# Kernel tuning notes

Hardware: AMD Instinct MI355X
Metric: run time of the kernel (lower is better)

## Reference

```python
import jax, jax.numpy as jnp
import numpy as np
from jax import lax

BASE = 10000.0

def _rope(x):
    # x: (b, h, w, c). Faithful to torch RoPE: angles depend only on one spatial
    # axis (h,k_max) and broadcast against the *w* axis of x (valid since h==w).
    b, h, w, c = x.shape
    k_max = c // 2
    theta = 1.0 / (BASE ** (jnp.arange(k_max, dtype=x.dtype) / k_max))  # (k_max,)
    angles = jnp.arange(h, dtype=x.dtype)[:, None] * theta              # (h, k_max)
    cos = jnp.cos(angles)[None, None]  # (1,1,h,k_max) -> broadcasts over w axis
    sin = jnp.sin(angles)[None, None]
    xr = x.reshape(b, h, w, k_max, 2)
    re, im = xr[..., 0], xr[..., 1]
    out = jnp.stack([re * cos - im * sin, re * sin + im * cos], axis=-1)
    return out.reshape(b, h, w, c)


def setup_inputs() -> dict:
    key = jax.random.key(0)
    k1, k2, k3 = jax.random.split(key, 3)
    B, C, H, W = 8, 128, 160, 160
    x = jax.random.normal(k1, (B, C, H, W), dtype=jnp.float32)
    qk_w = jax.random.normal(k2, (2 * C, C), dtype=jnp.float32) * 0.02
    qk_b = jnp.zeros((2 * C,), dtype=jnp.float32)
    lepe_w = jax.random.normal(k3, (C, 1, 3, 3), dtype=jnp.float32) * 0.1
    lepe_b = jnp.zeros((C,), dtype=jnp.float32)
    return {"x": x, "qk_w": qk_w, "qk_b": qk_b,
            "lepe_w": lepe_w, "lepe_b": lepe_b, "num_heads": 8}


def reference(x, qk_w, qk_b, lepe_w, lepe_b, num_heads):
    b, c, H, W = x.shape
    n = H * W
    hd = c // num_heads
    # raw row-major reshape (B,C,H,W) -> (B,N,C), matching torch .reshape
    xf = x.reshape(b, n, c)
    qk = (xf @ qk_w.T + qk_b).reshape(b, n, 2, c)
    q = jax.nn.elu(qk[:, :, 0]) + 1.0
    k = jax.nn.elu(qk[:, :, 1]) + 1.0
    v = xf
    q_rope = _rope(q.reshape(b, H, W, c)).reshape(b, n, num_heads, hd).transpose(0, 2, 1, 3)
    k_rope = _rope(k.reshape(b, H, W, c)).reshape(b, n, num_heads, hd).transpose(0, 2, 1, 3)
    qh = q.reshape(b, n, num_heads, hd).transpose(0, 2, 1, 3)  # (b,h,n,d)
    kh = k.reshape(b, n, num_heads, hd).transpose(0, 2, 1, 3)
    vh = v.reshape(b, n, num_heads, hd).transpose(0, 2, 1, 3)
    z = 1.0 / (jnp.einsum('bhnd,bhd->bhn', qh, kh.mean(axis=2)) + 1e-6)  # (b,h,n)
    scale = float(n) ** -0.5
    kv = jnp.einsum('bhnd,bhne->bhde', k_rope * scale, vh * scale)  # (b,h,d,d)
    out = jnp.einsum('bhnd,bhde->bhne', q_rope, kv) * z[..., None]  # (b,h,n,d)
    out = out.transpose(0, 2, 1, 3).reshape(b, n, c)
    # LePE: depthwise 3x3 conv on v laid out as image
    vimg = vh.transpose(0, 2, 1, 3).reshape(b, H, W, c).transpose(0, 3, 1, 2)  # (b,c,H,W)
    lepe = lax.conv_general_dilated(vimg, lepe_w, (1, 1), 'SAME',
                                    feature_group_count=c)
    lepe = lepe + lepe_b[None, :, None, None]
    out = out + lepe.transpose(0, 2, 3, 1).reshape(b, n, c)
    return out.transpose(0, 2, 1).reshape(b, c, H, W)
```

## Files before the change

kernel.cpp:

```cpp
#include <hip/hip_runtime.h>
#include <cstdint>
#include <cstddef>

#define NB 8
#define NC 128
#define NHH 160
#define NWW 160
#define NNN (NHH*NWW)
#define TILE_R 64
#define TPB (NNN/TILE_R)
#define NSLOTS 32
#define LN_B 0.14391156511f

typedef __attribute__((ext_vector_type(8))) short short8v;
typedef __attribute__((ext_vector_type(4))) short short4v;
typedef __attribute__((ext_vector_type(4))) float f32x4;
union B64x2 { short8v v8; short4v v4[2]; ushort u[8]; uint w[4]; };

__device__ __forceinline__ float elup1(float y){ return y>0.f? y+1.f : __expf(y); }
__device__ __forceinline__ ushort f2bf(float f){ uint x=__float_as_uint(f); x+=0x7fffu+((x>>16)&1u); return (ushort)(x>>16); }
__device__ __forceinline__ uint cvtpk(float lo, float hi){
  uint r;
  asm("v_cvt_pk_bf16_f32 %0, %1, %2" : "=v"(r) : "v"(lo), "v"(hi));
  return r;
}
__device__ __forceinline__ float frcp(float x){
  float r;
  asm("v_rcp_f32 %0, %1" : "=v"(r) : "v"(x));
  return r;
}
__device__ __forceinline__ float bfhi(uint u){ return __uint_as_float(u & 0xffff0000u); }
__device__ __forceinline__ float bflo(uint u){ return __uint_as_float(u << 16); }
__device__ __forceinline__ int divH(int i){ return ((i >> 5) * 6554) >> 15; }
__device__ __forceinline__ int iclamp(int v, int lo, int hi){ return v<lo?lo:(v>hi?hi:v); }

__global__ __launch_bounds__(256) void kprep(
    const float* __restrict__ qk_w, ushort* __restrict__ wbf,
    float2* __restrict__ rtab, float* __restrict__ zreg)
{
  const int id = blockIdx.x*256 + threadIdx.x;
  if (id < 2*NC*NC) wbf[id] = f2bf(qk_w[id]);
  if (id < NWW*64) {
    const int ww = id >> 6, f = id & 63;
    const float th = __expf(-LN_B * (float)f);
    float s, c; __sincosf((float)ww * th, &s, &c);
    rtab[id] = make_float2(c, s);
  }
  #pragma unroll
  for (int j = 0; j < 17; ++j)
    zreg[id + j*32768] = 0.f;
}

__global__ __launch_bounds__(256, 3) void k1_proj(
    const float* __restrict__ x, const ushort* __restrict__ wbf,
    const float* __restrict__ qk_b, const float2* __restrict__ rtab,
    float* __restrict__ kv_part, float* __restrict__ ksum_part)
{
  __shared__ __align__(16) ushort xbf[64][136];
  __shared__ __align__(16) ushort wch[64][136];
  __shared__ __align__(16) ushort xtp[64][68];
  __shared__ __align__(16) ushort krt[64][68];
  __shared__ float ksum_lds[NC];

  const int blk  = ((blockIdx.x & 7) * (NB*TPB/8)) + (blockIdx.x >> 3);
  const int b    = blk / TPB;
  const int tile = blk - b * TPB;
  const int i0   = tile * TILE_R;
  const int tid  = threadIdx.x;
  const int lane = tid & 63;
  const int wv   = tid >> 6;
  const int lg   = lane >> 4;
  const int ll   = lane & 15;
  const float* xb = x + (size_t)b*NNN*NC + (size_t)i0*NC;

  {
    const float4* src = (const float4*)xb;
    for (int f = tid; f < TILE_R*NC/4; f += 256) {
      float4 v = src[f];
      uint w0 = cvtpk(v.x, v.y), w1 = cvtpk(v.z, v.w);
      *(uint2*)&xbf[f >> 5][(f & 31) << 2] = make_uint2(w0, w1);
    }
  }
  if (tid < NC) ksum_lds[tid] = 0.f;
  __syncthreads();

  f32x4 kvacc[2];
  kvacc[0] = (f32x4){0.f,0.f,0.f,0.f};
  kvacc[1] = (f32x4){0.f,0.f,0.f,0.f};
  const int row0 = (wv<<4) + (lg<<2);

  int wfr4[4];
  #pragma unroll
  for (int r = 0; r < 4; ++r) {
    const int i = i0 + row0 + r;
    wfr4[r] = i - divH(i)*NWW;
  }

  for (int chunk = 0; chunk < 2; ++chunk) {
    if (chunk) __syncthreads();
    {
      const uint4* wsrc = (const uint4*)(wbf + (size_t)(NC + chunk*64)*NC);
      for (int f = tid; f < 1024; f += 256)
        *(uint4*)&wch[f >> 4][(f & 15) << 3] = wsrc[f];
    }
    {
      #pragma unroll
      for (int t = 0; t < 2; ++t) {
        const int task = tid + (t << 8);
        const int c = task & 63, rg = task >> 6;
        ushort tmp[8];
        #pragma unroll
        for (int k2 = 0; k2 < 8; ++k2) tmp[k2] = xbf[(rg<<3)+k2][(chunk<<6)+c];
        *(ushort4*)&xtp[c][(rg<<3)]   = make_ushort4(tmp[0],tmp[1],tmp[2],tmp[3]);
        *(ushort4*)&xtp[c][(rg<<3)+4] = make_ushort4(tmp[4],tmp[5],tmp[6],tmp[7]);
      }
    }
    __syncthreads();

    f32x4 acc[4];
    acc[0]=acc[1]=acc[2]=acc[3]=(f32x4){0.f,0.f,0.f,0.f};
    #pragma unroll
    for (int ks = 0; ks < 4; ++ks) {
      short8v a = *(const short8v*)&xbf[(wv<<4) + ll][(ks<<5) + (lg<<3)];
      #pragma unroll
      for (int nt = 0; nt < 4; ++nt) {
        short8v bb = *(const short8v*)&wch[(nt<<4) + ll][(ks<<5) + (lg<<3)];
        acc[nt] = __builtin_amdgcn_mfma_f32_16x16x32_bf16(a, bb, acc[nt], 0, 0, 0);
      }
    }

    #pragma unroll
    for (int nt = 0; nt < 4; ++nt) {
      const int kcl = (nt<<4) + ll;
      const int kc  = (chunk<<6) + kcl;
      const float bias = qk_b[NC + kc];
      float kk[4]; float ss = 0.f;
      #pragma unroll
      for (int r = 0; r < 4; ++r) { kk[r] = elup1(acc[nt][r] + bias); ss += kk[r]; }
      atomicAdd(&ksum_lds[kc], ss);
      ushort rb[4];
      #pragma unroll
      for (int r = 0; r < 4; ++r) {
        float p = __shfl_xor(kk[r], 1);
        float2 cs = rtab[wfr4[r]*64 + (kc >> 1)];
        float kr = (kc & 1) ? (p*cs.y + kk[r]*cs.x) : (kk[r]*cs.x - p*cs.y);
        rb[r] = f2bf(kr);
      }
      *(uint*)&krt[kcl][row0]   = (uint)rb[0] | ((uint)rb[1] << 16);
      *(uint*)&krt[kcl][row0+2] = (uint)rb[2] | ((uint)rb[3] << 16);
    }
    __syncthreads();

    #pragma unroll
    for (int ks = 0; ks < 2; ++ks) {
      const int rb2 = (ks<<5) + (lg<<3);
      B64x2 ua, ub;
      ua.v4[0] = *(const short4v*)&krt[(wv<<4) + ll][rb2];
      ua.v4[1] = *(const short4v*)&krt[(wv<<4) + ll][rb2+4];
      ub.v4[0] = *(const short4v*)&xtp[(wv<<4) + ll][rb2];
      ub.v4[1] = *(const short4v*)&xtp[(wv<<4) + ll][rb2+4];
      kvacc[chunk] = __builtin_amdgcn_mfma_f32_16x16x32_bf16(ua.v8, ub.v8, kvacc[chunk], 0, 0, 0);
    }
  }

  const int slot = blk & (NSLOTS-1);
  {
    float* kvp = kv_part + ((size_t)b*NSLOTS + slot) * 2048;
    #pragma unroll
    for (int e2 = 0; e2 < 2; ++e2) {
      const int h = (e2<<2) + wv;
      #pragma unroll
      for (int r = 0; r < 4; ++r) {
        const int d = (lg<<2) + r;
        atomicAdd(&kvp[(h<<8) + (d<<4) + ll], kvacc[e2][r]);
      }
    }
  }
  if (tid < NC) atomicAdd(&ksum_part[((size_t)b*NSLOTS + slot)*NC + tid], ksum_lds[tid]);
}

__global__ __launch_bounds__(256) void k_reduce(
    const float* __restrict__ kv_part, const float* __restrict__ ksum_part,
    float* __restrict__ kvf, float* __restrict__ kmean)
{
  const int gtid = blockIdx.x * 256 + threadIdx.x;
  const int b = gtid >> 11;
  const int cidx = gtid & 2047;
  float s = 0.f;
  for (int sl = 0; sl < NSLOTS; ++sl)
    s += kv_part[((size_t)b*NSLOTS + sl)*2048 + cidx];
  kvf[(size_t)b*2048 + cidx] = s * (1.f/25600.f);
  if (cidx < NC) {
    float t = 0.f;
    for (int sl = 0; sl < NSLOTS; ++sl)
      t += ksum_part[((size_t)b*NSLOTS + sl)*NC + cidx];
    kmean[(size_t)b*NC + cidx] = t * (1.f/25600.f);
  }
}

__global__ __launch_bounds__(256, 2) void k2_out(
    const float* __restrict__ x, const ushort* __restrict__ wbf,
    const float* __restrict__ qk_b, const float* __restrict__ kvf,
    const float* __restrict__ kmean, const float* __restrict__ lepe_w,
    const float* __restrict__ lepe_b, const float2* __restrict__ rtab,
    float* __restrict__ outp)
{
  __shared__ __align__(16) ushort qu_s[64*136];

  const int blk  = ((blockIdx.x & 7) * (NB*TPB/8)) + (blockIdx.x >> 3);
  const int b    = blk / TPB;
  const int tile = blk - b * TPB;
  const int i0   = tile * TILE_R;
  const int tid  = threadIdx.x;
  const int lane = tid & 63;
  const int wv   = tid >> 6;
  const int lg   = lane >> 4;
  const int ll   = lane & 15;
  const float* xb  = x + (size_t)b*NNN*NC;
  const float* xbt = xb + (size_t)i0*NC;

  f32x4 acc[8];
  #pragma unroll
  for (int t = 0; t < 8; ++t) acc[t] = (f32x4){0.f,0.f,0.f,0.f};
  #pragma unroll
  for (int ks = 0; ks < 4; ++ks) {
    const float* ap = xbt + (size_t)((wv<<4) + ll)*NC + (ks<<5) + (lg<<3);
    float4 a0 = *(const float4*)ap;
    float4 a1 = *(const float4*)(ap + 4);
    B64x2 af;
    af.w[0] = cvtpk(a0.x, a0.y); af.w[1] = cvtpk(a0.z, a0.w);
    af.w[2] = cvtpk(a1.x, a1.y); af.w[3] = cvtpk(a1.z, a1.w);
    #pragma unroll
    for (int nt = 0; nt < 8; ++nt) {
      short8v bb = *(const short8v*)(wbf + (size_t)((nt<<4) + ll)*NC + (ks<<5) + (lg<<3));
      acc[nt] = __builtin_amdgcn_mfma_f32_16x16x32_bf16(af.v8, bb, acc[nt], 0, 0, 0);
    }
  }

  const int row0 = (wv<<4) + (lg<<2);
  #pragma unroll
  for (int nt = 0; nt < 8; ++nt) {
    const int cg = (nt<<4) + ll;
    const float bias = qk_b[cg];
    #pragma unroll
    for (int r = 0; r < 4; ++r) {
      const int row = row0 + r;
      qu_s[row*136 + (cg ^ ((row & 7) << 3))] = f2bf(elup1(acc[nt][r] + bias));
    }
  }
  __syncthreads();

  const bool interior = (i0 >= 192) && (i0 <= NNN - 225);

  int wfa[4];
  #pragma unroll
  for (int mt = 0; mt < 4; ++mt) {
    const int i = i0 + (mt<<4) + ll;
    wfa[mt] = i - divH(i)*NWW;
  }

  #pragma unroll
  for (int hs = 0; hs < 2; ++hs) {
    const int h  = wv + (hs<<2);
    const int ch = (h<<4) + ll;
    B64x2 kb, kz;
    kb.v8 = (short8v){0,0,0,0,0,0,0,0};
    kz.v8 = (short8v){0,0,0,0,0,0,0,0};
    if (lg < 2) {
      const float* kvp = kvf + (size_t)b*2048 + (h<<8) + ll;
      #pragma unroll
      for (int j2 = 0; j2 < 4; ++j2) {
        float f0 = kvp[(((lg<<3) + 2*j2    ) << 4)];
        float f1 = kvp[(((lg<<3) + 2*j2 + 1) << 4)];
        kb.w[j2] = cvtpk(f0, f1);
      }
      const float* kmp = kmean + (size_t)b*NC + (h<<4) + (lg<<3);
      #pragma unroll
      for (int j2 = 0; j2 < 4; ++j2)
        kz.w[j2] = cvtpk(kmp[2*j2], kmp[2*j2+1]);
    }
    f32x4 pacc[4], zacc[4];
    #pragma unroll
    for (int mt = 0; mt < 4; ++mt) {
      short8v a  = (short8v){0,0,0,0,0,0,0,0};
      short8v au = (short8v){0,0,0,0,0,0,0,0};
      if (lg < 2) {
        const int row = (mt<<4) + ll;
        const int off = row*136 + ((((h<<1) + lg) ^ (row & 7)) << 3);
        B64x2 uq;
        uq.v8 = *(const short8v*)&qu_s[off];
        au = uq.v8;
        const float2* tp = rtab + wfa[mt]*64 + (h<<3) + (lg<<2);
        B64x2 ra;
        #pragma unroll
        for (int j = 0; j < 4; ++j) {
          float2 cs = tp[j];
          float e = bflo(uq.w[j]), o = bfhi(uq.w[j]);
          ra.w[j] = cvtpk(e*cs.x - o*cs.y, e*cs.y + o*cs.x);
        }
        a = ra.v8;
      }
      pacc[mt] = __builtin_amdgcn_mfma_f32_16x16x32_bf16(
          a,  kb.v8, (f32x4){0.f,0.f,0.f,0.f}, 0, 0, 0);
      zacc[mt] = __builtin_amdgcn_mfma_f32_16x16x32_bf16(
          au, kz.v8, (f32x4){0.f,0.f,0.f,0.f}, 0, 0, 0);
    }
    float wl[9];
    #pragma unroll
    for (int t = 0; t < 9; ++t) wl[t] = lepe_w[ch*9 + t];
    const float lb = lepe_b[ch];
    const float* xc = xb + ch;

    if (interior) {
      #pragma unroll
      for (int mt = 0; mt < 4; ++mt) {
        const int lrow = (mt<<4) + (lg<<2);
        const int ib   = i0 + lrow;
        const float* pu = xc + (size_t)(ib-161)*NC;
        const float* pm = xc + (size_t)(ib-1  )*NC;
        const float* pd = xc + (size_t)(ib+159)*NC;
        float mu[6], mm[6], md[6];
        #pragma unroll
        for (int j = 0; j < 6; ++j) {
          mu[j] = pu[j*NC]; mm[j] = pm[j*NC]; md[j] = pd[j*NC];
        }
        int ww = ib - divH(ib)*NWW;
        float4 ov;
        #pragma unroll
        for (int r = 0; r < 4; ++r) {
          const float zz = frcp(zacc[mt][r] + 1e-6f);
          const float fx0 = ww > 0   ? 1.f : 0.f;
          const float fx2 = ww < 159 ? 1.f : 0.f;
          float lp = lb;
          lp += fx0*(wl[0]*mu[r] + wl[3]*mm[r] + wl[6]*md[r]);
          lp +=     (wl[1]*mu[r+1] + wl[4]*mm[r+1] + wl[7]*md[r+1]);
          lp += fx2*(wl[2]*mu[r+2] + wl[5]*mm[r+2] + wl[8]*md[r+2]);
          (&ov.x)[r] = pacc[mt][r]*zz + lp;
          ww = (ww == NWW-1) ? 0 : ww + 1;
        }
        *(float4*)(outp + ((size_t)b*NC + ch)*NNN + ib) = ov;
      }
    } else {
      #pragma unroll
      for (int mt = 0; mt < 4; ++mt) {
        const int lrow = (mt<<4) + (lg<<2);
        const int ib   = i0 + lrow;
        float mu[6], mm[6], md[6];
        #pragma unroll
        for (int j = 0; j < 6; ++j) {
          const int im = ib - 1 + j;
          mu[j] = xc[(size_t)(iclamp(im-160, 0, NNN-1)) * NC];
          mm[j] = xc[(size_t)(iclamp(im,     0, NNN-1)) * NC];
          md[j] = xc[(size_t)(iclamp(im+160, 0, NNN-1)) * NC];
        }
        int hh = divH(ib);
        int ww = ib - hh*NWW;
        float4 ov;
        #pragma unroll
        for (int r = 0; r < 4; ++r) {
          const float zz = frcp(zacc[mt][r] + 1e-6f);
          const float fy0 = hh > 0   ? 1.f : 0.f;
          const float fy2 = hh < 159 ? 1.f : 0.f;
          const float fx0 = ww > 0   ? 1.f : 0.f;
          const float fx2 = ww < 159 ? 1.f : 0.f;
          float lp = lb;
          lp += fy0*(fx0*wl[0]*mu[r] + wl[1]*mu[r+1] + fx2*wl[2]*mu[r+2]);
          lp +=     (fx0*wl[3]*mm[r] + wl[4]*mm[r+1] + fx2*wl[5]*mm[r+2]);
          lp += fy2*(fx0*wl[6]*md[r] + wl[7]*md[r+1] + fx2*wl[8]*md[r+2]);
          (&ov.x)[r] = pacc[mt][r]*zz + lp;
          const int cy = (ww == NWW-1) ? 1 : 0;
          hh += cy;
          ww = cy ? 0 : ww + 1;
        }
        *(float4*)(outp + ((size_t)b*NC + ch)*NNN + ib) = ov;
      }
    }
  }
}

extern "C" void kernel_launch(void* const* d_in, const int* in_sizes, int n_in,
                              void* d_out, int out_size, void* d_ws, size_t ws_size,
                              hipStream_t stream) {
  const float* x      = (const float*)d_in[0];
  const float* qk_w   = (const float*)d_in[1];
  const float* qk_b   = (const float*)d_in[2];
  const float* lepe_w = (const float*)d_in[3];
  const float* lepe_b = (const float*)d_in[4];
  float* outp = (float*)d_out;

  float* kv_part   = (float*)d_ws;
  float* ksum_part = kv_part + (size_t)NB*NSLOTS*2048;
  float* kvf       = ksum_part + (size_t)NB*NSLOTS*NC;
  float* kmean     = kvf + (size_t)NB*2048;
  float2* rtab     = (float2*)(kmean + (size_t)NB*NC);
  ushort* wbf      = (ushort*)(rtab + (size_t)NWW*64);

  hipLaunchKernelGGL(kprep, dim3(128), dim3(256), 0, stream,
                     qk_w, wbf, rtab, kv_part);
  hipLaunchKernelGGL(k1_proj, dim3(NB*TPB), dim3(256), 0, stream,
                     x, wbf, qk_b, rtab, kv_part, ksum_part);
  hipLaunchKernelGGL(k_reduce, dim3(64), dim3(256), 0, stream,
                     kv_part, ksum_part, kvf, kmean);
  hipLaunchKernelGGL(k2_out, dim3(NB*TPB), dim3(256), 0, stream,
                     x, wbf, qk_b, kvf, kmean, lepe_w, lepe_b, rtab, outp);
}
```

Baseline: 191.7 us.

## Compute Q projection in k1 and pass bf16 Q to k2 via workspace

The pass that computes K now also computes the Q half of the projection (four chunks instead of two) and writes elu(Q)+1 as bf16 to a global scratch buffer. The output kernel loads this precomputed Q tile into LDS instead of reading fp32 x and recomputing the Q GEMM. This moves the Q GEMM into the first kernel and trades one fp32 read of x in k2 for a bf16 write plus a bf16 read of Q (about 52MB of extra traffic). The Q stores in k1 are scattered 2-byte writes, which may coalesce poorly.

```diff
diff --git a/kernel.cpp b/kernel.cpp
--- a/kernel.cpp
+++ b/kernel.cpp
@@ -54,7 +54,8 @@
 __global__ __launch_bounds__(256, 3) void k1_proj(
     const float* __restrict__ x, const ushort* __restrict__ wbf,
     const float* __restrict__ qk_b, const float2* __restrict__ rtab,
-    float* __restrict__ kv_part, float* __restrict__ ksum_part)
+    ushort* __restrict__ qu, float* __restrict__ kv_part,
+    float* __restrict__ ksum_part)
 {
   __shared__ __align__(16) ushort xbf[64][136];
   __shared__ __align__(16) ushort wch[64][136];
@@ -96,21 +97,21 @@
     wfr4[r] = i - divH(i)*NWW;
   }
 
-  for (int chunk = 0; chunk < 2; ++chunk) {
+  for (int chunk = 0; chunk < 4; ++chunk) {
     if (chunk) __syncthreads();
     {
-      const uint4* wsrc = (const uint4*)(wbf + (size_t)(NC + chunk*64)*NC);
+      const uint4* wsrc = (const uint4*)(wbf + (size_t)(chunk*64)*NC);
       for (int f = tid; f < 1024; f += 256)
         *(uint4*)&wch[f >> 4][(f & 15) << 3] = wsrc[f];
     }
-    {
+    if (chunk >= 2) {
       #pragma unroll
       for (int t = 0; t < 2; ++t) {
         const int task = tid + (t << 8);
         const int c = task & 63, rg = task >> 6;
         ushort tmp[8];
         #pragma unroll
-        for (int k2 = 0; k2 < 8; ++k2) tmp[k2] = xbf[(rg<<3)+k2][(chunk<<6)+c];
+        for (int k2 = 0; k2 < 8; ++k2) tmp[k2] = xbf[(rg<<3)+k2][((chunk-2)<<6)+c];
         *(ushort4*)&xtp[c][(rg<<3)]   = make_ushort4(tmp[0],tmp[1],tmp[2],tmp[3]);
         *(ushort4*)&xtp[c][(rg<<3)+4] = make_ushort4(tmp[4],tmp[5],tmp[6],tmp[7]);
       }
@@ -129,37 +130,50 @@
       }
     }
 
-    #pragma unroll
-    for (int nt = 0; nt < 4; ++nt) {
-      const int kcl = (nt<<4) + ll;
-      const int kc  = (chunk<<6) + kcl;
-      const float bias = qk_b[NC + kc];
-      float kk[4]; float ss = 0.f;
-      #pragma unroll
-      for (int r = 0; r < 4; ++r) { kk[r] = elup1(acc[nt][r] + bias); ss += kk[r]; }
-      atomicAdd(&ksum_lds[kc], ss);
-      ushort rb[4];
-      #pragma unroll
-      for (int r = 0; r < 4; ++r) {
-        float p = __shfl_xor(kk[r], 1);
-        float2 cs = rtab[wfr4[r]*64 + (kc >> 1)];
-        float kr = (kc & 1) ? (p*cs.y + kk[r]*cs.x) : (kk[r]*cs.x - p*cs.y);
-        rb[r] = f2bf(kr);
-      }
-      *(uint*)&krt[kcl][row0]   = (uint)rb[0] | ((uint)rb[1] << 16);
-      *(uint*)&krt[kcl][row0+2] = (uint)rb[2] | ((uint)rb[3] << 16);
-    }
-    __syncthreads();
-
-    #pragma unroll
-    for (int ks = 0; ks < 2; ++ks) {
-      const int rb2 = (ks<<5) + (lg<<3);
-      B64x2 ua, ub;
-      ua.v4[0] = *(const short4v*)&krt[(wv<<4) + ll][rb2];
-      ua.v4[1] = *(const short4v*)&krt[(wv<<4) + ll][rb2+4];
-      ub.v4[0] = *(const short4v*)&xtp[(wv<<4) + ll][rb2];
-      ub.v4[1] = *(const short4v*)&xtp[(wv<<4) + ll][rb2+4];
-      kvacc[chunk] = __builtin_amdgcn_mfma_f32_16x16x32_bf16(ua.v8, ub.v8, kvacc[chunk], 0, 0, 0);
+    if (chunk < 2) {
+      ushort* qb = qu + ((size_t)b*NNN + (size_t)i0)*NC;
+      #pragma unroll
+      for (int nt = 0; nt < 4; ++nt) {
+        const int cg = (chunk<<6) + (nt<<4) + ll;
+        const float bias = qk_b[cg];
+        #pragma unroll
+        for (int r = 0; r < 4; ++r)
+          qb[(size_t)(row0 + r)*NC + cg] = f2bf(elup1(acc[nt][r] + bias));
+      }
+    } else {
+      #pragma unroll
+      for (int nt = 0; nt < 4; ++nt) {
+        const int kcl = (nt<<4) + ll;
+        const int kc  = ((chunk-2)<<6) + kcl;
+        const float bias = qk_b[NC + kc];
+        float kk[4]; float ss = 0.f;
+        #pragma unroll
+        for (int r = 0; r < 4; ++r) { kk[r] = elup1(acc[nt][r] + bias); ss += kk[r]; }
+        atomicAdd(&ksum_lds[kc], ss);
+        ushort rb[4];
+        #pragma unroll
+        for (int r = 0; r < 4; ++r) {
+          float p = __shfl_xor(kk[r], 1);
+          float2 cs = rtab[wfr4[r]*64 + (kc >> 1)];
+          float kr = (kc & 1) ? (p*cs.y + kk[r]*cs.x) : (kk[r]*cs.x - p*cs.y);
+          rb[r] = f2bf(kr);
+        }
+        *(uint*)&krt[kcl][row0]   = (uint)rb[0] | ((uint)rb[1] << 16);
+        *(uint*)&krt[kcl][row0+2] = (uint)rb[2] | ((uint)rb[3] << 16);
+      }
+      __syncthreads();
+
+      const int e2 = chunk - 2;
+      #pragma unroll
+      for (int ks = 0; ks < 2; ++ks) {
+        const int rb2 = (ks<<5) + (lg<<3);
+        B64x2 ua, ub;
+        ua.v4[0] = *(const short4v*)&krt[(wv<<4) + ll][rb2];
+        ua.v4[1] = *(const short4v*)&krt[(wv<<4) + ll][rb2+4];
+        ub.v4[0] = *(const short4v*)&xtp[(wv<<4) + ll][rb2];
+        ub.v4[1] = *(const short4v*)&xtp[(wv<<4) + ll][rb2+4];
+        kvacc[e2] = __builtin_amdgcn_mfma_f32_16x16x32_bf16(ua.v8, ub.v8, kvacc[e2], 0, 0, 0);
+      }
     }
   }
 
@@ -199,11 +213,10 @@
 }
 
 __global__ __launch_bounds__(256, 2) void k2_out(
-    const float* __restrict__ x, const ushort* __restrict__ wbf,
-    const float* __restrict__ qk_b, const float* __restrict__ kvf,
-    const float* __restrict__ kmean, const float* __restrict__ lepe_w,
-    const float* __restrict__ lepe_b, const float2* __restrict__ rtab,
-    float* __restrict__ outp)
+    const float* __restrict__ x, const ushort* __restrict__ qu,
+    const float* __restrict__ kvf, const float* __restrict__ kmean,
+    const float* __restrict__ lepe_w, const float* __restrict__ lepe_b,
+    const float2* __restrict__ rtab, float* __restrict__ outp)
 {
   __shared__ __align__(16) ushort qu_s[64*136];
 
@@ -216,36 +229,16 @@
   const int wv   = tid >> 6;
   const int lg   = lane >> 4;
   const int ll   = lane & 15;
-  const float* xb  = x + (size_t)b*NNN*NC;
-  const float* xbt = xb + (size_t)i0*NC;
-
-  f32x4 acc[8];
-  #pragma unroll
-  for (int t = 0; t < 8; ++t) acc[t] = (f32x4){0.f,0.f,0.f,0.f};
-  #pragma unroll
-  for (int ks = 0; ks < 4; ++ks) {
-    const float* ap = xbt + (size_t)((wv<<4) + ll)*NC + (ks<<5) + (lg<<3);
-    float4 a0 = *(const float4*)ap;
-    float4 a1 = *(const float4*)(ap + 4);
-    B64x2 af;
-    af.w[0] = cvtpk(a0.x, a0.y); af.w[1] = cvtpk(a0.z, a0.w);
-    af.w[2] = cvtpk(a1.x, a1.y); af.w[3] = cvtpk(a1.z, a1.w);
+  const float* xb = x + (size_t)b*NNN*NC;
+
+  {
+    const uint4* qsrc = (const uint4*)(qu + ((size_t)b*NNN + (size_t)i0)*NC);
     #pragma unroll
-    for (int nt = 0; nt < 8; ++nt) {
-      short8v bb = *(const short8v*)(wbf + (size_t)((nt<<4) + ll)*NC + (ks<<5) + (lg<<3));
-      acc[nt] = __builtin_amdgcn_mfma_f32_16x16x32_bf16(af.v8, bb, acc[nt], 0, 0, 0);
-    }
-  }
-
-  const int row0 = (wv<<4) + (lg<<2);
-  #pragma unroll
-  for (int nt = 0; nt < 8; ++nt) {
-    const int cg = (nt<<4) + ll;
-    const float bias = qk_b[cg];
-    #pragma unroll
-    for (int r = 0; r < 4; ++r) {
-      const int row = row0 + r;
-      qu_s[row*136 + (cg ^ ((row & 7) << 3))] = f2bf(elup1(acc[nt][r] + bias));
+    for (int t = 0; t < 4; ++t) {
+      const int f = tid + (t << 8);
+      uint4 v = qsrc[f];
+      const int row = f >> 4, c8 = f & 15;
+      *(uint4*)&qu_s[row*136 + ((c8 ^ (row & 7)) << 3)] = v;
     }
   }
   __syncthreads();
@@ -394,13 +387,14 @@
   float* kmean     = kvf + (size_t)NB*2048;
   float2* rtab     = (float2*)(kmean + (size_t)NB*NC);
   ushort* wbf      = (ushort*)(rtab + (size_t)NWW*64);
+  ushort* qubuf    = wbf + (size_t)2*NC*NC;
 
   hipLaunchKernelGGL(kprep, dim3(128), dim3(256), 0, stream,
                      qk_w, wbf, rtab, kv_part);
   hipLaunchKernelGGL(k1_proj, dim3(NB*TPB), dim3(256), 0, stream,
-                     x, wbf, qk_b, rtab, kv_part, ksum_part);
+                     x, wbf, qk_b, rtab, qubuf, kv_part, ksum_part);
   hipLaunchKernelGGL(k_reduce, dim3(64), dim3(256), 0, stream,
                      kv_part, ksum_part, kvf, kmean);
   hipLaunchKernelGGL(k2_out, dim3(NB*TPB), dim3(256), 0, stream,
-                     x, wbf, qk_b, kvf, kmean, lepe_w, lepe_b, rtab, outp);
-}
+                     x, qubuf, kvf, kmean, lepe_w, lepe_b, rtab, outp);
+}
```

New measurement: 164.5 us. 1.17x faster.
